# Optimization experiments

Hardware: AMD Instinct MI355X
Metric: run time of the kernel (lower is better)

## Reference

```python
import jax, jax.numpy as jnp
import numpy as np

N = 768
C = 1024            # box_head representation size
HID = 256           # RePN hidden / gcn_hidden
HEADS1 = 4
K = 5               # topk neighbors
NEG_SLOPE = 0.2


def setup_inputs() -> dict:
    key = jax.random.key(0)
    ks = jax.random.split(key, 24)
    feats = jax.random.normal(ks[0], (N, C), dtype=jnp.float32)
    # valid boxes: x0<x1, y0<y1 inside an 800x800 image
    xy = jax.random.uniform(ks[1], (N, 2), dtype=jnp.float32) * 600.0
    wh = jax.random.uniform(ks[2], (N, 2), dtype=jnp.float32) * 150.0 + 2.0
    boxes = jnp.concatenate([xy, xy + wh], axis=1)
    s = 0.02
    # RePN fc1 weight [2C+4, HID] split into f1 / f2 / geom blocks (same math as concat)
    W1_f1 = jax.random.normal(ks[3], (C, HID), jnp.float32) * s
    W1_f2 = jax.random.normal(ks[4], (C, HID), jnp.float32) * s
    W1_g = jax.random.normal(ks[5], (4, HID), jnp.float32) * s
    b1 = jax.random.normal(ks[6], (HID,), jnp.float32) * s
    W2r = jax.random.normal(ks[7], (HID, 1), jnp.float32) * s
    b2r = jax.random.normal(ks[8], (1,), jnp.float32) * s
    # GAT1: (C+4) -> HID per head, 4 heads
    Wg1 = jax.random.normal(ks[9], (C + 4, HEADS1 * HID), jnp.float32) * s
    asrc1 = jax.random.normal(ks[10], (HEADS1, HID), jnp.float32) * s
    adst1 = jax.random.normal(ks[11], (HEADS1, HID), jnp.float32) * s
    bg1 = jax.random.normal(ks[12], (HEADS1 * HID,), jnp.float32) * s
    # GAT2: 4*HID -> 2, 1 head
    Wg2 = jax.random.normal(ks[13], (HEADS1 * HID, 2), jnp.float32) * s
    asrc2 = jax.random.normal(ks[14], (1, 2), jnp.float32) * s
    adst2 = jax.random.normal(ks[15], (1, 2), jnp.float32) * s
    bg2 = jax.random.normal(ks[16], (2,), jnp.float32) * s
    Wb1 = jax.random.normal(ks[17], (HEADS1 * HID + 4, HID // 2), jnp.float32) * s
    bb1 = jax.random.normal(ks[18], (HID // 2,), jnp.float32) * s
    Wb2 = jax.random.normal(ks[19], (HID // 2, 4), jnp.float32) * s
    bb2 = jax.random.normal(ks[20], (4,), jnp.float32) * s
    return {"feats": feats, "boxes": boxes, "img_h": 800, "img_w": 800,
            "W1_f1": W1_f1, "W1_f2": W1_f2, "W1_g": W1_g, "b1": b1,
            "W2r": W2r, "b2r": b2r,
            "Wg1": Wg1, "asrc1": asrc1, "adst1": adst1, "bg1": bg1,
            "Wg2": Wg2, "asrc2": asrc2, "adst2": adst2, "bg2": bg2,
            "Wb1": Wb1, "bb1": bb1, "Wb2": Wb2, "bb2": bb2}


def _box_geom(boxes, h, w):
    x0 = boxes[:, 0] / w
    y0 = boxes[:, 1] / h
    x1 = boxes[:, 2] / w
    y1 = boxes[:, 3] / h
    return jnp.stack([x0, y0, x1 - x0, y1 - y0], axis=1)


def _repn(feats, boxes, W1_f1, W1_f2, W1_g, b1, W2r, b2r):
    # fc1(cat([f1, f2, |b1-b2|])) decomposed as three matmuls (identical math).
    fa = feats @ W1_f1                          # [N, HID] contribution of row feature
    fb = feats @ W1_f2                          # [N, HID] contribution of col feature
    geom = jnp.abs(boxes[:, None, :] - boxes[None, :, :])  # [N, N, 4]
    h = jax.nn.relu(fa[:, None, :] + fb[None, :, :] + geom @ W1_g + b1)  # [N, N, HID]
    return (h @ W2r)[..., 0] + b2r[0]           # [N, N]


def _make_edges(rel):
    n = rel.shape[0]
    rn = rel - jnp.eye(n, dtype=rel.dtype) * 1e6
    _, idx = jax.lax.top_k(rn, K)               # [N, K] top-k neighbors per node
    dst = jnp.repeat(jnp.arange(n), K)
    src_row = dst                               # edge_index[0] in the torch code
    dst_row = idx.reshape(-1)                   # edge_index[1]
    # PyG GATConv default add_self_loops=True
    loops = jnp.arange(n)
    return jnp.concatenate([src_row, loops]), jnp.concatenate([dst_row, loops])


def _gat(x, e_src, e_dst, W, a_src, a_dst, bias, heads, out_c):
    n = x.shape[0]
    h = (x @ W).reshape(n, heads, out_c)        # [N, H, F]
    alpha_s = jnp.einsum('nhf,hf->nh', h, a_src)
    alpha_d = jnp.einsum('nhf,hf->nh', h, a_dst)
    e = alpha_s[e_src] + alpha_d[e_dst]         # [E, H]
    e = jax.nn.leaky_relu(e, NEG_SLOPE)
    m = jax.ops.segment_max(e, e_dst, num_segments=n)       # [N, H]
    ex = jnp.exp(e - m[e_dst])
    denom = jax.ops.segment_sum(ex, e_dst, num_segments=n)  # [N, H]
    attn = ex / denom[e_dst]
    msg = h[e_src] * attn[..., None]            # [E, H, F]
    out = jax.ops.segment_sum(msg, e_dst, num_segments=n)   # [N, H, F]
    return out.reshape(n, heads * out_c) + bias


def reference(feats, boxes, img_h, img_w,
              W1_f1, W1_f2, W1_g, b1, W2r, b2r,
              Wg1, asrc1, adst1, bg1, Wg2, asrc2, adst2, bg2,
              Wb1, bb1, Wb2, bb2):
    h_f = jnp.float32(img_h)
    w_f = jnp.float32(img_w)
    geom = _box_geom(boxes, h_f, w_f)                       # [N, 4]
    x = jnp.concatenate([feats, geom], axis=1)              # [N, C+4]
    rel = _repn(feats, boxes, W1_f1, W1_f2, W1_g, b1, W2r, b2r)
    e_src, e_dst = _make_edges(rel)
    h1 = jax.nn.relu(_gat(x, e_src, e_dst, Wg1, asrc1, adst1, bg1, HEADS1, HID))
    logits = _gat(h1, e_src, e_dst, Wg2, asrc2, adst2, bg2, 1, 2)  # [N, 2]
    prob_miss = jax.nn.softmax(logits, axis=1)[:, 1]
    reg_in = jnp.concatenate([h1, geom], axis=1)
    delta = jax.nn.relu(reg_in @ Wb1 + bb1) @ Wb2 + bb2     # [N, 4]
    px0, py0, px1, py1 = boxes[:, 0], boxes[:, 1], boxes[:, 2], boxes[:, 3]
    pw = px1 - px0
    ph = py1 - py0
    pcx = px0 + 0.5 * pw
    pcy = py0 + 0.5 * ph
    dx, dy, dw, dh = delta[:, 0], delta[:, 1], delta[:, 2], delta[:, 3]
    gcx = dx * pw + pcx
    gcy = dy * ph + pcy
    gw = jnp.exp(dw) * pw
    gh = jnp.exp(dh) * ph
    final_boxes = jnp.stack([gcx - 0.5 * gw, gcy - 0.5 * gh,
                             gcx + 0.5 * gw, gcy + 0.5 * gh], axis=1)
    # pack all outputs into one array: [N, N + 2 + 4 + 1]
    return jnp.concatenate([rel, logits, final_boxes, prob_miss[:, None]], axis=1)
```

## Files before the change

kernel.cpp:

```cpp
#include <hip/hip_runtime.h>
#include <hip/hip_fp16.h>
#include <float.h>

#define NN   768
#define CC   1024
#define HIDD 256
#define NH1  4
#define TOPK 5
#define NEDG (NN*TOPK + NN)
#define XW   (CC+4)
#define KP   1056
#define OUTW (NN+7)
#define G1W  (NH1*HIDD)
#define RH   128

typedef __attribute__((ext_vector_type(8))) short short8;
typedef __attribute__((ext_vector_type(4))) float f32x4;

__device__ unsigned short g_featsb[NN*CC];
__device__ unsigned short g_xb[NN*KP];
__device__ unsigned short g_wg1t[G1W*KP];
__device__ unsigned short g_w1f1t[HIDD*CC];
__device__ unsigned short g_w1f2t[HIDD*CC];
__device__ unsigned short g_wb1t[RH*KP];
__device__ unsigned short g_reginb[NN*KP];
__device__ __half g_fah[NN*HIDD];
__device__ __half g_fbh[NN*HIDD];
__device__ __half2 g_wrel[5*128];
__device__ __half g_relph[8*NN*NN];
__device__ float g_hg[NN*G1W];
__device__ float g_as1[NN*NH1], g_ad1[NN*NH1];
__device__ int   g_idx[NN*TOPK];
__device__ int   g_off[NN+1], g_inlist[NEDG];
__device__ float g_h2[NN*2], g_as2[NN], g_ad2[NN];
__device__ float g_r1p[3*NN*RH];

__device__ __forceinline__ unsigned short f2bf(float f){
    unsigned int u = __float_as_uint(f);
    unsigned int r = (u + 0x7FFFu + ((u >> 16) & 1u)) >> 16;
    return (unsigned short)r;
}
__device__ __forceinline__ int edge_src(int eid){
    return (eid < NN*TOPK) ? (eid / TOPK) : (eid - NN*TOPK);
}
__device__ __forceinline__ __half2 h2max(__half2 a, __half2 b){
    __half2 r;
    asm("v_pk_max_f16 %0, %1, %2" : "=v"(r) : "v"(a), "v"(b));
    return r;
}

__device__ __forceinline__ void tconv(const float* __restrict__ W, int Kin, int N, int Kpad,
                                      unsigned short* __restrict__ O, int k0, int n0,
                                      int tx, int ty, float (*tile)[33]){
    #pragma unroll
    for (int i = 0; i < 4; i++){
        int k = k0 + ty + 8*i;
        tile[ty+8*i][tx] = (k < Kin) ? W[(size_t)k*N + n0 + tx] : 0.f;
    }
    __syncthreads();
    #pragma unroll
    for (int i = 0; i < 4; i++){
        int n = n0 + ty + 8*i;
        O[(size_t)n*Kpad + k0 + tx] = f2bf(tile[tx][ty+8*i]);
    }
}

__global__ void __launch_bounds__(256) k_prep_all(const float* __restrict__ feats,
                                                  const float* __restrict__ boxes,
                                                  const int* __restrict__ ih,
                                                  const int* __restrict__ iw,
                                                  const float* __restrict__ Wg1,
                                                  const float* __restrict__ W1f1,
                                                  const float* __restrict__ W1f2,
                                                  const float* __restrict__ Wb1,
                                                  const float* __restrict__ W1g,
                                                  const float* __restrict__ W2r){
    __shared__ float tile[32][33];
    int b = blockIdx.x, t = threadIdx.x;
    if (b < 384){
        int idx = b*256 + t;
        int n = idx >> 7, c8 = (idx & 127) << 3;
        const float* src = &feats[(size_t)n*CC + c8];
        float4 v0 = *(const float4*)src;
        float4 v1 = *(const float4*)(src + 4);
        uint4 pk;
        pk.x = (unsigned)f2bf(v0.x) | ((unsigned)f2bf(v0.y) << 16);
        pk.y = (unsigned)f2bf(v0.z) | ((unsigned)f2bf(v0.w) << 16);
        pk.z = (unsigned)f2bf(v1.x) | ((unsigned)f2bf(v1.y) << 16);
        pk.w = (unsigned)f2bf(v1.z) | ((unsigned)f2bf(v1.w) << 16);
        *(uint4*)&g_featsb[(size_t)n*CC + c8] = pk;
        *(uint4*)&g_xb[(size_t)n*KP + c8] = pk;
        return;
    }
    if (b < 387){
        int n = (b - 384)*256 + t;
        float w = (float)iw[0], h = (float)ih[0];
        float x0 = boxes[n*4+0]/w, y0 = boxes[n*4+1]/h;
        float x1 = boxes[n*4+2]/w, y1 = boxes[n*4+3]/h;
        float ge[4] = {x0, y0, x1-x0, y1-y0};
        #pragma unroll
        for (int c = 0; c < 4; c++){
            unsigned short bv = f2bf(ge[c]);
            g_xb[(size_t)n*KP + CC + c] = bv;
            g_reginb[(size_t)n*KP + CC + c] = bv;
        }
        for (int c = 4; c < KP - CC; c++){
            g_xb[(size_t)n*KP + CC + c] = 0;
            g_reginb[(size_t)n*KP + CC + c] = 0;
        }
        return;
    }
    if (b == 2087){
        for (int e = t; e < 5*128; e += 256){
            int r = e >> 7, fp = e & 127;
            const float* src = (r < 4) ? &W1g[r*HIDD + 2*fp] : &W2r[2*fp];
            g_wrel[e] = __floats2half2_rn(src[0], src[1]);
        }
        return;
    }
    int bb = b - 387;
    int tx = t & 31, ty = t >> 5;
    if (bb < 1056){
        int kt = bb % 33, nt = bb / 33;
        tconv(Wg1, XW, G1W, KP, g_wg1t, kt*32, nt*32, tx, ty, tile);
    } else if (bb < 1312){
        int b2 = bb - 1056;
        tconv(W1f1, CC, HIDD, CC, g_w1f1t, (b2%32)*32, (b2/32)*32, tx, ty, tile);
    } else if (bb < 1568){
        int b2 = bb - 1312;
        tconv(W1f2, CC, HIDD, CC, g_w1f2t, (b2%32)*32, (b2/32)*32, tx, ty, tile);
    } else {
        int b2 = bb - 1568;
        tconv(Wb1, XW, RH, KP, g_wb1t, (b2%33)*32, (b2/33)*32, tx, ty, tile);
    }
}

#define LSTR 40
__device__ __forceinline__ void mfma_gemm64(const unsigned short* __restrict__ A, int lda,
                                            const unsigned short* __restrict__ Bt, int ldb,
                                            int kstart, int Ks, float* __restrict__ Cf,
                                            __half* __restrict__ Ch, int ldc,
                                            const float* __restrict__ bias, bool relu,
                                            int bm, int bn,
                                            unsigned short* As, unsigned short* Bs){
    const int t = threadIdx.x;
    const int l = t & 63, w = t >> 6;
    const int wr = w >> 1, wc = w & 1;
    const int sr = t >> 2, sq = (t & 3) * 8;
    const size_t aoff = (size_t)(bm + sr)*lda + sq + (size_t)kstart*32;
    const size_t boff = (size_t)(bn + sr)*ldb + sq + (size_t)kstart*32;

    f32x4 acc[2][2];
    #pragma unroll
    for (int i = 0; i < 2; i++)
        #pragma unroll
        for (int j = 0; j < 2; j++)
            acc[i][j] = (f32x4){0.f,0.f,0.f,0.f};

    const int arow0 = (wr*32 + (l & 15)) * LSTR + ((l >> 4) * 8);
    const int brow0 = (wc*32 + (l & 15)) * LSTR + ((l >> 4) * 8);

    float4 a0v, b0v, a1v, b1v;
    a0v = *(const float4*)&A[aoff];            b0v = *(const float4*)&Bt[boff];
    a1v = *(const float4*)&A[aoff + 32];       b1v = *(const float4*)&Bt[boff + 32];

    for (int s = 0; s < Ks; s += 2){
        *(float4*)&As[sr*LSTR + sq] = a0v;
        *(float4*)&Bs[sr*LSTR + sq] = b0v;
        if (s + 2 < Ks){
            a0v = *(const float4*)&A[aoff + (size_t)(s+2)*32];
            b0v = *(const float4*)&Bt[boff + (size_t)(s+2)*32];
        }
        __syncthreads();
        {
            short8 fa0 = *(const short8*)&As[arow0];
            short8 fa1 = *(const short8*)&As[arow0 + 16*LSTR];
            short8 fb0 = *(const short8*)&Bs[brow0];
            short8 fb1 = *(const short8*)&Bs[brow0 + 16*LSTR];
            acc[0][0] = __builtin_amdgcn_mfma_f32_16x16x32_bf16(fa0, fb0, acc[0][0], 0, 0, 0);
            acc[0][1] = __builtin_amdgcn_mfma_f32_16x16x32_bf16(fa0, fb1, acc[0][1], 0, 0, 0);
            acc[1][0] = __builtin_amdgcn_mfma_f32_16x16x32_bf16(fa1, fb0, acc[1][0], 0, 0, 0);
            acc[1][1] = __builtin_amdgcn_mfma_f32_16x16x32_bf16(fa1, fb1, acc[1][1], 0, 0, 0);
        }
        __syncthreads();
        if (s + 1 >= Ks) break;
        *(float4*)&As[64*LSTR + sr*LSTR + sq] = a1v;
        *(float4*)&Bs[64*LSTR + sr*LSTR + sq] = b1v;
        if (s + 3 < Ks){
            a1v = *(const float4*)&A[aoff + (size_t)(s+3)*32];
            b1v = *(const float4*)&Bt[boff + (size_t)(s+3)*32];
        }
        __syncthreads();
        {
            short8 fa0 = *(const short8*)&As[64*LSTR + arow0];
            short8 fa1 = *(const short8*)&As[64*LSTR + arow0 + 16*LSTR];
            short8 fb0 = *(const short8*)&Bs[64*LSTR + brow0];
            short8 fb1 = *(const short8*)&Bs[64*LSTR + brow0 + 16*LSTR];
            acc[0][0] = __builtin_amdgcn_mfma_f32_16x16x32_bf16(fa0, fb0, acc[0][0], 0, 0, 0);
            acc[0][1] = __builtin_amdgcn_mfma_f32_16x16x32_bf16(fa0, fb1, acc[0][1], 0, 0, 0);
            acc[1][0] = __builtin_amdgcn_mfma_f32_16x16x32_bf16(fa1, fb0, acc[1][0], 0, 0, 0);
            acc[1][1] = __builtin_amdgcn_mfma_f32_16x16x32_bf16(fa1, fb1, acc[1][1], 0, 0, 0);
        }
        __syncthreads();
    }

    #pragma unroll
    for (int mi = 0; mi < 2; mi++){
        #pragma unroll
        for (int nj = 0; nj < 2; nj++){
            int col  = bn + wc*32 + nj*16 + (l & 15);
            int row0 = bm + wr*32 + mi*16 + ((l >> 4) * 4);
            float bv = bias ? bias[col] : 0.f;
            #pragma unroll
            for (int r = 0; r < 4; r++){
                float v = acc[mi][nj][r] + bv;
                if (relu) v = fmaxf(v, 0.f);
                if (Ch) Ch[(size_t)(row0+r)*ldc + col] = __float2half(v);
                else    Cf[(size_t)(row0+r)*ldc + col] = v;
            }
        }
    }
}

__global__ void __launch_bounds__(256) k_gemm_all(const float* __restrict__ b1){
    __shared__ unsigned short As[2*64*LSTR];
    __shared__ unsigned short Bs[2*64*LSTR];
    int b = blockIdx.x;
    if (b < 192){
        mfma_gemm64(g_xb, KP, g_wg1t, KP, 0, 33, g_hg, nullptr, G1W, nullptr, false,
                    (b>>4)*64, (b&15)*64, As, Bs);
    } else if (b < 240){
        int bb = b - 192;
        mfma_gemm64(g_featsb, CC, g_w1f1t, CC, 0, 32, nullptr, g_fah, HIDD, b1, false,
                    (bb>>2)*64, (bb&3)*64, As, Bs);
    } else {
        int bb = b - 240;
        mfma_gemm64(g_featsb, CC, g_w1f2t, CC, 0, 32, nullptr, g_fbh, HIDD, nullptr, false,
                    (bb>>2)*64, (bb&3)*64, As, Bs);
    }
}

__global__ void __launch_bounds__(256) k_gemm_r1(){
    __shared__ unsigned short As[2*64*LSTR];
    __shared__ unsigned short Bs[2*64*LSTR];
    int b = blockIdx.x;
    int slice = b / 24, bb = b % 24;
    mfma_gemm64(g_reginb, KP, g_wb1t, KP, slice*11, 11,
                g_r1p + (size_t)slice*NN*RH, nullptr, RH, nullptr, false,
                (bb>>1)*64, (bb&1)*64, As, Bs);
}

#define RSUB 32
__global__ void __launch_bounds__(256) __attribute__((amdgpu_waves_per_eu(4, 4)))
k_rel(const float* __restrict__ boxes){
    __shared__ __half2 sfa[16][68];
    __shared__ __half2 sfb[16][68];
    const int t = threadIdx.x;
    const int ib = blockIdx.y*64, jb = blockIdx.x*64;
    const int fc0 = blockIdx.z*RSUB;
    const int fpbase = blockIdx.z*16;
    const int rg = t >> 4, cg = t & 15;

    {
        const int fp = t & 15, nq = t >> 4;
        #pragma unroll
        for (int a2 = 0; a2 < 4; a2++){
            int node = nq*4 + a2;
            sfa[fp][node] = *(const __half2*)&g_fah[(size_t)(ib+node)*HIDD + fc0 + 2*fp];
            sfb[fp][node] = *(const __half2*)&g_fbh[(size_t)(jb+node)*HIDD + fc0 + 2*fp];
        }
    }

    float4 bi[4], bj[4];
    #pragma unroll
    for (int a = 0; a < 4; a++) bi[a] = *(const float4*)&boxes[(ib + rg*4 + a)*4];
    #pragma unroll
    for (int b = 0; b < 4; b++) bj[b] = *(const float4*)&boxes[(jb + cg*4 + b)*4];
    __half2 gg[4][4][4];
    #pragma unroll
    for (int a = 0; a < 4; a++)
        #pragma unroll
        for (int b = 0; b < 4; b++){
            const float* pa = (const float*)&bi[a];
            const float* pb = (const float*)&bj[b];
            #pragma unroll
            for (int c = 0; c < 4; c++){
                float gv = fabsf(pa[c] - pb[c]);
                gg[a][b][c] = __floats2half2_rn(gv, gv);
            }
        }
    __syncthreads();

    const __half2 hz = __floats2half2_rn(0.f, 0.f);
    __half2 acc2[4][4];
    #pragma unroll
    for (int a = 0; a < 4; a++)
        #pragma unroll
        for (int b = 0; b < 4; b++) acc2[a][b] = hz;

    #pragma unroll 4
    for (int fp = 0; fp < 16; fp++){
        __half2 w0  = g_wrel[0*128 + fpbase + fp];
        __half2 w1  = g_wrel[1*128 + fpbase + fp];
        __half2 w2  = g_wrel[2*128 + fpbase + fp];
        __half2 w3  = g_wrel[3*128 + fpbase + fp];
        __half2 wrv = g_wrel[4*128 + fpbase + fp];
        float4 fa_raw = *(const float4*)&sfa[fp][rg*4];
        float4 fb_raw = *(const float4*)&sfb[fp][cg*4];
        const __half2* FA = (const __half2*)&fa_raw;
        const __half2* FB = (const __half2*)&fb_raw;
        #pragma unroll
        for (int a = 0; a < 4; a++)
            #pragma unroll
            for (int b = 0; b < 4; b++){
                __half2 s = __hadd2(FA[a], FB[b]);
                s = __hfma2(gg[a][b][0], w0, s);
                s = __hfma2(gg[a][b][1], w1, s);
                s = __hfma2(gg[a][b][2], w2, s);
                s = __hfma2(gg[a][b][3], w3, s);
                s = h2max(s, hz);
                acc2[a][b] = __hfma2(s, wrv, acc2[a][b]);
            }
    }

    __half* po = g_relph + (size_t)blockIdx.z*NN*NN + (size_t)ib*NN + jb;
    #pragma unroll
    for (int a = 0; a < 4; a++){
        unsigned short u[4];
        #pragma unroll
        for (int b = 0; b < 4; b++){
            float sum = __low2float(acc2[a][b]) + __high2float(acc2[a][b]);
            u[b] = __half_as_ushort(__float2half(sum));
        }
        uint2 o;
        o.x = (unsigned)u[0] | ((unsigned)u[1] << 16);
        o.y = (unsigned)u[2] | ((unsigned)u[3] << 16);
        *(uint2*)&po[(size_t)(rg*4+a)*NN + cg*4] = o;
    }
}

__global__ void __launch_bounds__(64) k_topk(const float* __restrict__ asrc,
                                             const float* __restrict__ adst,
                                             const float* __restrict__ b2r,
                                             float* __restrict__ out){
    int i = blockIdx.x, t = threadIdx.x;
    float* row = out + (size_t)i*OUTW;

    float ss[4] = {0,0,0,0}, sd[4] = {0,0,0,0};
    const float* hrow = g_hg + (size_t)i*G1W;
    #pragma unroll
    for (int k = 0; k < 16; k++){
        const int h = k >> 2;
        int u = t + 64*k;
        float hv = hrow[u];
        ss[h] += hv * asrc[u];
        sd[h] += hv * adst[u];
    }
    #pragma unroll
    for (int h = 0; h < 4; h++)
        for (int off = 32; off; off >>= 1){
            ss[h] += __shfl_down(ss[h], off);
            sd[h] += __shfl_down(sd[h], off);
        }
    if (t == 0){
        #pragma unroll
        for (int h = 0; h < 4; h++){ g_as1[i*4+h] = ss[h]; g_ad1[i*4+h] = sd[h]; }
    }

    const __half* p0 = g_relph + (size_t)i*NN;
    float bb = b2r[0];
    float rv[12];
    #pragma unroll
    for (int kk = 0; kk < 6; kk++){
        int j2 = 128*kk + 2*t;
        float sx = bb, sy = bb;
        #pragma unroll
        for (int z = 0; z < 8; z++){
            __half2 hv = *(const __half2*)&p0[(size_t)z*NN*NN + j2];
            sx += __low2float(hv);
            sy += __high2float(hv);
        }
        rv[2*kk]   = sx;
        rv[2*kk+1] = sy;
        row[j2]   = sx;
        row[j2+1] = sy;
    }

    int sel[TOPK];
    for (int k = 0; k < TOPK; k++){
        float bv = -FLT_MAX; int bj = NN;
        #pragma unroll
        for (int kk = 0; kk < 12; kk++){
            int j = 128*(kk >> 1) + 2*t + (kk & 1);
            if (j == i) continue;
            bool used = false;
            #pragma unroll
            for (int u = 0; u < TOPK; u++) if (u < k && sel[u] == j) used = true;
            if (used) continue;
            float v = rv[kk];
            if (v > bv || (v == bv && j < bj)){ bv = v; bj = j; }
        }
        for (int off = 32; off; off >>= 1){
            float v2 = __shfl_down(bv, off);
            int   j2 = __shfl_down(bj, off);
            if (v2 > bv || (v2 == bv && j2 < bj)){ bv = v2; bj = j2; }
        }
        bv = __shfl(bv, 0); bj = __shfl(bj, 0);
        sel[k] = bj;
    }
    if (t < TOPK) g_idx[i*TOPK + t] = sel[t];
}

__global__ void __launch_bounds__(1024) k_csr(){
    __shared__ int sa[NN], sb[NN];
    int t = threadIdx.x;
    for (int i = t; i < NN; i += 1024) sa[i] = 0;
    __syncthreads();
    for (int e = t; e < NEDG; e += 1024){
        int d = (e < NN*TOPK) ? g_idx[e] : (e - NN*TOPK);
        atomicAdd(&sa[d], 1);
    }
    __syncthreads();
    int* src = sa; int* dst = sb;
    for (int off = 1; off < NN; off <<= 1){
        for (int i = t; i < NN; i += 1024)
            dst[i] = src[i] + ((i >= off) ? src[i-off] : 0);
        __syncthreads();
        int* tmp = src; src = dst; dst = tmp;
    }
    for (int i = t; i < NN; i += 1024) g_off[i] = (i ? src[i-1] : 0);
    if (t == 0) g_off[NN] = src[NN-1];
    for (int i = t; i < NN; i += 1024) dst[i] = 0;
    __syncthreads();
    for (int e = t; e < NEDG; e += 1024){
        int d = (e < NN*TOPK) ? g_idx[e] : (e - NN*TOPK);
        int pos = atomicAdd(&dst[d], 1);
        int base = d ? src[d-1] : 0;
        g_inlist[base + pos] = e;
    }
}

__global__ void __launch_bounds__(256) k_gat1(const float* __restrict__ bg1,
                                              const float* __restrict__ Wg2,
                                              const float* __restrict__ as2w,
                                              const float* __restrict__ ad2w){
    __shared__ float sattn[NN*4];
    __shared__ float sden[4];
    __shared__ float sp0[4], sp1[4];
    int n = blockIdx.x, t = threadIdx.x;
    int beg = g_off[n], deg = g_off[n+1] - beg;
    int w = t >> 6, l = t & 63;

    {
        float adn = g_ad1[n*NH1 + w];
        float s = 0.f;
        for (int e = l; e < deg; e += 64){
            int src = edge_src(g_inlist[beg + e]);
            float ev = g_as1[src*NH1 + w] + adn;
            ev = (ev > 0.f) ? ev : 0.2f*ev;
            float ex = expf(ev);
            sattn[e*4 + w] = ex;
            s += ex;
        }
        for (int off = 32; off; off >>= 1) s += __shfl_down(s, off);
        if (l == 0) sden[w] = s;
    }
    __syncthreads();

    float rd[NH1];
    #pragma unroll
    for (int h = 0; h < NH1; h++) rd[h] = 1.f / sden[h];
    float acc[NH1] = {0.f,0.f,0.f,0.f};
    for (int e = 0; e < deg; e++){
        int src = edge_src(g_inlist[beg + e]);
        const float* hr = g_hg + (size_t)src*G1W;
        #pragma unroll
        for (int h = 0; h < NH1; h++)
            acc[h] += sattn[e*4 + h] * hr[h*HIDD + t];
    }
    float p0 = 0.f, p1 = 0.f;
    #pragma unroll
    for (int h = 0; h < NH1; h++){
        int c = h*HIDD + t;
        float v = acc[h]*rd[h] + bg1[c];
        v = fmaxf(v, 0.f);
        g_reginb[(size_t)n*KP + c] = f2bf(v);
        p0 += v * Wg2[c*2 + 0];
        p1 += v * Wg2[c*2 + 1];
    }
    for (int off = 32; off; off >>= 1){
        p0 += __shfl_down(p0, off);
        p1 += __shfl_down(p1, off);
    }
    if (l == 0){ sp0[w] = p0; sp1[w] = p1; }
    __syncthreads();
    if (t == 0){
        float h0 = sp0[0]+sp0[1]+sp0[2]+sp0[3];
        float h1 = sp1[0]+sp1[1]+sp1[2]+sp1[3];
        g_h2[n*2+0] = h0; g_h2[n*2+1] = h1;
        g_as2[n] = h0*as2w[0] + h1*as2w[1];
        g_ad2[n] = h0*ad2w[0] + h1*ad2w[1];
    }
}

__global__ void __launch_bounds__(64) k_tail(const float* __restrict__ bg2,
                                             const float* __restrict__ Wb2,
                                             const float* __restrict__ bb1,
                                             const float* __restrict__ bb2,
                                             const float* __restrict__ boxes,
                                             float* __restrict__ out){
    int n = blockIdx.x, t = threadIdx.x;

    int beg = g_off[n], deg = g_off[n+1] - beg;
    float adn = g_ad2[n];
    float den = 0.f, l0 = 0.f, l1 = 0.f;
    for (int e = t; e < deg; e += 64){
        int src = edge_src(g_inlist[beg + e]);
        float ev = g_as2[src] + adn;
        ev = (ev > 0.f) ? ev : 0.2f*ev;
        float ex = expf(ev);
        den += ex;
        l0 += ex * g_h2[src*2+0];
        l1 += ex * g_h2[src*2+1];
    }
    #pragma unroll
    for (int off = 32; off; off >>= 1){
        den += __shfl_xor(den, off);
        l0  += __shfl_xor(l0, off);
        l1  += __shfl_xor(l1, off);
    }

    float d0 = 0.f, d1 = 0.f, d2 = 0.f, d3 = 0.f;
    const float* q0 = g_r1p + (size_t)n*RH;
    #pragma unroll
    for (int kk = 0; kk < 2; kk++){
        int k = t + 64*kk;
        float r = q0[k] + q0[k + (size_t)NN*RH] + q0[k + 2*(size_t)NN*RH] + bb1[k];
        r = fmaxf(r, 0.f);
        float4 wv = *(const float4*)&Wb2[k*4];
        d0 += r*wv.x; d1 += r*wv.y; d2 += r*wv.z; d3 += r*wv.w;
    }
    #pragma unroll
    for (int off = 32; off; off >>= 1){
        d0 += __shfl_xor(d0, off);
        d1 += __shfl_xor(d1, off);
        d2 += __shfl_xor(d2, off);
        d3 += __shfl_xor(d3, off);
    }

    if (t == 0){
        float rdv = 1.f / den;
        float L0 = l0*rdv + bg2[0];
        float L1 = l1*rdv + bg2[1];
        out[(size_t)n*OUTW + NN + 0] = L0;
        out[(size_t)n*OUTW + NN + 1] = L1;
        float m = fmaxf(L0, L1);
        float e0 = expf(L0 - m), e1 = expf(L1 - m);
        out[(size_t)n*OUTW + NN + 6] = e1 / (e0 + e1);

        float dd0 = d0 + bb2[0], dd1 = d1 + bb2[1];
        float dd2 = d2 + bb2[2], dd3 = d3 + bb2[3];
        float px0 = boxes[n*4+0], py0 = boxes[n*4+1];
        float px1 = boxes[n*4+2], py1 = boxes[n*4+3];
        float pw = px1 - px0, ph = py1 - py0;
        float pcx = px0 + 0.5f*pw, pcy = py0 + 0.5f*ph;
        float gcx = dd0*pw + pcx, gcy = dd1*ph + pcy;
        float gw = expf(dd2)*pw,  gh = expf(dd3)*ph;
        out[(size_t)n*OUTW + NN + 2] = gcx - 0.5f*gw;
        out[(size_t)n*OUTW + NN + 3] = gcy - 0.5f*gh;
        out[(size_t)n*OUTW + NN + 4] = gcx + 0.5f*gw;
        out[(size_t)n*OUTW + NN + 5] = gcy + 0.5f*gh;
    }
}

extern "C" void kernel_launch(void* const* d_in, const int* in_sizes, int n_in,
                              void* d_out, int out_size, void* d_ws, size_t ws_size,
                              hipStream_t stream){
    const float* feats = (const float*)d_in[0];
    const float* boxes = (const float*)d_in[1];
    const int*   ih    = (const int*)  d_in[2];
    const int*   iw    = (const int*)  d_in[3];
    const float* W1f1  = (const float*)d_in[4];
    const float* W1f2  = (const float*)d_in[5];
    const float* W1g   = (const float*)d_in[6];
    const float* b1    = (const float*)d_in[7];
    const float* W2r   = (const float*)d_in[8];
    const float* b2r   = (const float*)d_in[9];
    const float* Wg1   = (const float*)d_in[10];
    const float* asrc1 = (const float*)d_in[11];
    const float* adst1 = (const float*)d_in[12];
    const float* bg1   = (const float*)d_in[13];
    const float* Wg2   = (const float*)d_in[14];
    const float* asrc2 = (const float*)d_in[15];
    const float* adst2 = (const float*)d_in[16];
    const float* bg2   = (const float*)d_in[17];
    const float* Wb1   = (const float*)d_in[18];
    const float* bb1   = (const float*)d_in[19];
    const float* Wb2   = (const float*)d_in[20];
    const float* bb2   = (const float*)d_in[21];
    float* out = (float*)d_out;

    k_prep_all<<<2088, 256, 0, stream>>>(feats, boxes, ih, iw, Wg1, W1f1, W1f2, Wb1, W1g, W2r);
    k_gemm_all<<<288, 256, 0, stream>>>(b1);
    k_rel<<<dim3(NN/64, NN/64, 8), 256, 0, stream>>>(boxes);
    k_topk<<<NN, 64, 0, stream>>>(asrc1, adst1, b2r, out);
    k_csr<<<1, 1024, 0, stream>>>();
    k_gat1<<<NN, 256, 0, stream>>>(bg1, Wg2, asrc2, adst2);
    k_gemm_r1<<<72, 256, 0, stream>>>();
    k_tail<<<NN, 64, 0, stream>>>(bg2, Wb2, bb1, bb2, boxes, out);
}
```

Measured before the change: 94.39 us.

## Split-K the fused GEMM launch into two halves and reduce partials downstream

```diff
diff --git a/kernel.cpp b/kernel.cpp
--- a/kernel.cpp
+++ b/kernel.cpp
@@ -24,10 +24,11 @@
 __device__ unsigned short g_w1f2t[HIDD*CC];
 __device__ unsigned short g_wb1t[RH*KP];
 __device__ unsigned short g_reginb[NN*KP];
-__device__ __half g_fah[NN*HIDD];
-__device__ __half g_fbh[NN*HIDD];
+__device__ __half g_fahp[2*NN*HIDD];
+__device__ __half g_fbhp[2*NN*HIDD];
 __device__ __half2 g_wrel[5*128];
 __device__ __half g_relph[8*NN*NN];
+__device__ float g_hgp[2*NN*G1W];
 __device__ float g_hg[NN*G1W];
 __device__ float g_as1[NN*NH1], g_ad1[NN*NH1];
 __device__ int   g_idx[NN*TOPK];
@@ -226,16 +227,28 @@
     __shared__ unsigned short As[2*64*LSTR];
     __shared__ unsigned short Bs[2*64*LSTR];
     int b = blockIdx.x;
-    if (b < 192){
-        mfma_gemm64(g_xb, KP, g_wg1t, KP, 0, 33, g_hg, nullptr, G1W, nullptr, false,
-                    (b>>4)*64, (b&15)*64, As, Bs);
-    } else if (b < 240){
-        int bb = b - 192;
-        mfma_gemm64(g_featsb, CC, g_w1f1t, CC, 0, 32, nullptr, g_fah, HIDD, b1, false,
+    if (b < 384){
+        int p = b >> 7 >> 1;
+        p = (b >= 192) ? 1 : 0;
+        int bb = b - p*192;
+        int ks = p ? 17 : 0, Ks = p ? 16 : 17;
+        mfma_gemm64(g_xb, KP, g_wg1t, KP, ks, Ks,
+                    g_hgp + (size_t)p*NN*G1W, nullptr, G1W, nullptr, false,
+                    (bb>>4)*64, (bb&15)*64, As, Bs);
+    } else if (b < 480){
+        int q = b - 384;
+        int p = (q >= 48) ? 1 : 0;
+        int bb = q - p*48;
+        mfma_gemm64(g_featsb, CC, g_w1f1t, CC, p*16, 16,
+                    nullptr, g_fahp + (size_t)p*NN*HIDD, HIDD,
+                    p ? nullptr : b1, false,
                     (bb>>2)*64, (bb&3)*64, As, Bs);
     } else {
-        int bb = b - 240;
-        mfma_gemm64(g_featsb, CC, g_w1f2t, CC, 0, 32, nullptr, g_fbh, HIDD, nullptr, false,
+        int q = b - 480;
+        int p = (q >= 48) ? 1 : 0;
+        int bb = q - p*48;
+        mfma_gemm64(g_featsb, CC, g_w1f2t, CC, p*16, 16,
+                    nullptr, g_fbhp + (size_t)p*NN*HIDD, HIDD, nullptr, false,
                     (bb>>2)*64, (bb&3)*64, As, Bs);
     }
 }
@@ -266,8 +279,12 @@
         #pragma unroll
         for (int a2 = 0; a2 < 4; a2++){
             int node = nq*4 + a2;
-            sfa[fp][node] = *(const __half2*)&g_fah[(size_t)(ib+node)*HIDD + fc0 + 2*fp];
-            sfb[fp][node] = *(const __half2*)&g_fbh[(size_t)(jb+node)*HIDD + fc0 + 2*fp];
+            size_t o = (size_t)(ib+node)*HIDD + fc0 + 2*fp;
+            size_t o2 = (size_t)(jb+node)*HIDD + fc0 + 2*fp;
+            sfa[fp][node] = __hadd2(*(const __half2*)&g_fahp[o],
+                                    *(const __half2*)&g_fahp[o + (size_t)NN*HIDD]);
+            sfb[fp][node] = __hadd2(*(const __half2*)&g_fbhp[o2],
+                                    *(const __half2*)&g_fbhp[o2 + (size_t)NN*HIDD]);
         }
     }
 
@@ -347,12 +364,15 @@
     float* row = out + (size_t)i*OUTW;
 
     float ss[4] = {0,0,0,0}, sd[4] = {0,0,0,0};
-    const float* hrow = g_hg + (size_t)i*G1W;
+    const float* hp0 = g_hgp + (size_t)i*G1W;
+    const float* hp1 = hp0 + (size_t)NN*G1W;
+    float* hout = g_hg + (size_t)i*G1W;
     #pragma unroll
     for (int k = 0; k < 16; k++){
         const int h = k >> 2;
         int u = t + 64*k;
-        float hv = hrow[u];
+        float hv = hp0[u] + hp1[u];
+        hout[u] = hv;
         ss[h] += hv * asrc[u];
         sd[h] += hv * adst[u];
     }
@@ -601,7 +621,7 @@
     float* out = (float*)d_out;
 
     k_prep_all<<<2088, 256, 0, stream>>>(feats, boxes, ih, iw, Wg1, W1f1, W1f2, Wb1, W1g, W2r);
-    k_gemm_all<<<288, 256, 0, stream>>>(b1);
+    k_gemm_all<<<576, 256, 0, stream>>>(b1);
     k_rel<<<dim3(NN/64, NN/64, 8), 256, 0, stream>>>(boxes);
     k_topk<<<NN, 64, 0, stream>>>(asrc1, adst1, b2r, out);
     k_csr<<<1, 1024, 0, stream>>>();
```

Result: no change. 94.48 us (+0.1%).
